# Performance work log

Measured on AMD Instinct MI355X. Metric: run time of the kernel, lower is better.

The kernel has to match this reference:

```python
import jax, jax.numpy as jnp
import numpy as np

NUM_SONGS = 2000
N1 = NUM_SONGS + 1  # incl. padding idx 0
EMB = 64
B = 32
S = 5    # num_prev_shows
M = 25   # max_songs_per_show


def setup_inputs() -> dict:
    key = jax.random.key(0)
    ks = jax.random.split(key, 32)
    def lin(k, i, o):
        kw, kb = jax.random.split(k)
        s = 1.0 / np.sqrt(i)
        return (jax.random.uniform(kw, (i, o), jnp.float32, -s, s),
                jax.random.uniform(kb, (o,), jnp.float32, -s, s))
    song_emb = jax.random.normal(ks[0], (N1, EMB), jnp.float32)
    song_emb = song_emb.at[0].set(0.0)  # padding_idx=0
    gcn_w1, gcn_b1 = lin(ks[1], EMB, EMB)
    gcn_w2, gcn_b2 = lin(ks[2], EMB, EMB)
    q_w, q_b = lin(ks[3], EMB, EMB)
    k_w, k_b = lin(ks[4], EMB, EMB)
    v_w, v_b = lin(ks[5], EMB, EMB)
    venue_t = jax.random.normal(ks[6], (200, EMB // 4), jnp.float32)
    tour_t = jax.random.normal(ks[7], (20, EMB // 4), jnp.float32)
    country_t = jax.random.normal(ks[8], (50, EMB // 8), jnp.float32)
    fest_t = jax.random.normal(ks[9], (2, EMB // 8), jnp.float32)
    mara_t = jax.random.normal(ks[10], (2, EMB // 8), jnp.float32)
    ctx_in = EMB // 2 + 3 * (EMB // 8)  # 56
    ctx_w, ctx_b = lin(ks[11], ctx_in, EMB)
    p1_w, p1_b = lin(ks[12], EMB * 3, EMB * 2)
    p2_w, p2_b = lin(ks[13], EMB * 2, EMB)
    p3_w, p3_b = lin(ks[14], EMB, 1)
    return {
        'song_ids': jax.random.randint(ks[20], (B,), 0, N1),
        'prev_setlists': jax.random.randint(ks[21], (B, S, M), 0, N1),
        'venue_ids': jax.random.randint(ks[22], (B,), 0, 200),
        'tour_ids': jax.random.randint(ks[23], (B,), 0, 20),
        'country_ids': jax.random.randint(ks[24], (B,), 0, 50),
        'is_festival': jax.random.randint(ks[25], (B,), 0, 2),
        'is_marathon': jax.random.randint(ks[26], (B,), 0, 2),
        'song_emb': song_emb,
        'gcn_w1': gcn_w1, 'gcn_b1': gcn_b1, 'gcn_w2': gcn_w2, 'gcn_b2': gcn_b2,
        'q_w': q_w, 'q_b': q_b, 'k_w': k_w, 'k_b': k_b, 'v_w': v_w, 'v_b': v_b,
        'venue_t': venue_t, 'tour_t': tour_t, 'country_t': country_t,
        'fest_t': fest_t, 'mara_t': mara_t,
        'ctx_w': ctx_w, 'ctx_b': ctx_b,
        'p1_w': p1_w, 'p1_b': p1_b, 'p2_w': p2_w, 'p2_b': p2_b,
        'p3_w': p3_w, 'p3_b': p3_b,
    }


def _build_adj(prev_setlists):
    # co-occurrence counts via one scatter-add (replaces nested python loops)
    b, s, m = prev_setlists.shape
    mask = prev_setlists > 0
    pair_ok = (mask[:, :, :, None] & mask[:, :, None, :]
               & ~jnp.eye(m, dtype=bool))  # exclude same position i==j
    flat_idx = (prev_setlists[:, :, :, None] * N1
                + prev_setlists[:, :, None, :]).reshape(b, -1)
    w = pair_ok.astype(jnp.float32).reshape(b, -1)
    adj = jnp.zeros((b, N1 * N1), jnp.float32)
    adj = adj.at[jnp.arange(b)[:, None], flat_idx].add(w)
    adj = adj.reshape(b, N1, N1)
    return adj / (adj.sum(axis=2, keepdims=True) + 1e-10)


def _forward(song_ids, prev_setlists, venue_ids, tour_ids, country_ids,
             is_festival, is_marathon, song_emb, gcn_w1, gcn_b1, gcn_w2,
             gcn_b2, q_w, q_b, k_w, k_b, v_w, v_b, venue_t, tour_t,
             country_t, fest_t, mara_t, ctx_w, ctx_b, p1_w, p1_b, p2_w,
             p2_b, p3_w, p3_b):
    b = song_ids.shape[0]
    adj = _build_adj(prev_setlists)                      # [B,N1,N1]
    x = jnp.broadcast_to(song_emb[None], (b, N1, EMB))   # [B,N1,E]
    for w_, b_ in ((gcn_w1, gcn_b1), (gcn_w2, gcn_b2)):
        agg = jnp.einsum('bnm,bme->bne', adj, x)
        x = jax.nn.relu(agg @ w_ + b_)
    song_embs = x
    # ragged masked-mean show embeddings
    mask = (prev_setlists > 0).astype(jnp.float32)       # [B,S,M]
    gathered = jax.vmap(lambda se, ids: se[ids])(song_embs, prev_setlists)  # [B,S,M,E]
    cnt = mask.sum(-1, keepdims=True)                    # [B,S,1]
    show_embs = jnp.where(cnt > 0,
                          (gathered * mask[..., None]).sum(2) / jnp.maximum(cnt, 1.0),
                          0.0)                           # [B,S,E]
    ctx = jnp.concatenate([venue_t[venue_ids], tour_t[tour_ids],
                           country_t[country_ids], fest_t[is_festival],
                           mara_t[is_marathon]], axis=-1)
    ctx = ctx @ ctx_w + ctx_b                            # [B,E]
    # temporal attention
    q = ctx @ q_w + q_b                                  # [B,E]
    k = show_embs @ k_w + k_b                            # [B,S,E]
    v = show_embs @ v_w + v_b
    scores = jnp.einsum('be,bse->bs', q, k) / jnp.sqrt(jnp.float32(EMB))
    attn = jax.nn.softmax(scores, axis=-1)
    attended = jnp.einsum('bs,bse->be', attn, v)
    cand = song_embs[jnp.arange(b), song_ids]
    h = jnp.concatenate([cand, ctx, attended], axis=-1)  # [B,3E]
    h = jax.nn.relu(h @ p1_w + p1_b)   # dropout is eval-mode identity
    h = jax.nn.relu(h @ p2_w + p2_b)
    logits = (h @ p3_w + p3_b).squeeze(-1)
    return jax.nn.sigmoid(logits)


def reference(song_ids, prev_setlists, venue_ids, tour_ids, country_ids,
              is_festival, is_marathon, song_emb, gcn_w1, gcn_b1, gcn_w2,
              gcn_b2, q_w, q_b, k_w, k_b, v_w, v_b, venue_t, tour_t,
              country_t, fest_t, mara_t, ctx_w, ctx_b, p1_w, p1_b, p2_w,
              p2_b, p3_w, p3_b):
    return _forward(song_ids, prev_setlists, venue_ids, tour_ids,
                    country_ids, is_festival, is_marathon, song_emb,
                    gcn_w1, gcn_b1, gcn_w2, gcn_b2, q_w, q_b, k_w, k_b,
                    v_w, v_b, venue_t, tour_t, country_t, fest_t, mara_t,
                    ctx_w, ctx_b, p1_w, p1_b, p2_w, p2_b, p3_w, p3_b)
```

## Files before the change

kernel.cpp:

```cpp
#include <hip/hip_runtime.h>

#define N1    2001
#define EMB   64
#define NSHOW 5
#define MSONG 25
#define NPOS  (NSHOW * MSONG)
#define MAXU  128
#define NT    1024
#define WT    68

__global__ __launch_bounds__(NT)
__attribute__((amdgpu_waves_per_eu(4, 4)))
void setsgnn_kernel(
    const int* __restrict__ song_ids,
    const int* __restrict__ prev_setlists,
    const int* __restrict__ venue_ids,
    const int* __restrict__ tour_ids,
    const int* __restrict__ country_ids,
    const int* __restrict__ is_festival,
    const int* __restrict__ is_marathon,
    const float* __restrict__ song_emb,
    const float* __restrict__ gcn_w1, const float* __restrict__ gcn_b1,
    const float* __restrict__ gcn_w2, const float* __restrict__ gcn_b2,
    const float* __restrict__ q_w,  const float* __restrict__ q_b,
    const float* __restrict__ k_w,  const float* __restrict__ k_b,
    const float* __restrict__ v_w,  const float* __restrict__ v_b,
    const float* __restrict__ venue_t, const float* __restrict__ tour_t,
    const float* __restrict__ country_t, const float* __restrict__ fest_t,
    const float* __restrict__ mara_t,
    const float* __restrict__ ctx_w, const float* __restrict__ ctx_b,
    const float* __restrict__ p1_w,  const float* __restrict__ p1_b,
    const float* __restrict__ p2_w,  const float* __restrict__ p2_b,
    const float* __restrict__ p3_w,  const float* __restrict__ p3_b,
    float* __restrict__ out)
{
    const int b    = blockIdx.x;
    const int tid  = threadIdx.x;
    const int wv   = tid >> 6;
    const int lane = tid & 63;
    const int col0 = tid & 63;
    const int eq0  = tid >> 6;

    __shared__ __align__(16) float xb0[MAXU][EMB];
    __shared__ __align__(16) float wldsT[2][EMB][WT];
    __shared__ __align__(16) float blds[2][EMB];
    __shared__ __align__(16) float bias_ctx[EMB], bias_q[EMB], bias_k[EMB], bias_v[EMB];
    __shared__ __align__(16) float bias_p1[128], bias_p2[EMB], bias_p3w[EMB];
    __shared__ float bias_p3b;
    __shared__ int   idmap[N1];
    __shared__ int   sl[NPOS];
    __shared__ int   pmap[NPOS];
    __shared__ int   list_ids[MAXU];
    __shared__ float c_us[MAXU][NSHOW];
    __shared__ float occv[MAXU];
    __shared__ float invv[MAXU];
    __shared__ float cntm1[NSHOW];
    __shared__ float invc[NSHOW];
    __shared__ int   U_cnt;
    __shared__ __align__(16) float Xsum[NSHOW][EMB];
    __shared__ float XW[NSHOW][EMB];
    __shared__ float ctxin[56];
    __shared__ float ctxv[EMB];
    __shared__ float qv[EMB];
    __shared__ float vatt[NSHOW][EMB];
    __shared__ float attnw[NSHOW];
    __shared__ float hbuf[3 * EMB];
    __shared__ float h1b[128];
    __shared__ float partial[NT];

    float w1r[4], w2r[4];
    #pragma unroll
    for (int j = 0; j < 4; j++) w1r[j] = gcn_w1[(eq0 * 4 + j) * EMB + col0];
    #pragma unroll
    for (int j = 0; j < 4; j++) w2r[j] = gcn_w2[(eq0 * 4 + j) * EMB + col0];
    float4 bb;
    if (tid < 32) bb = (tid < 16) ? ((const float4*)gcn_b1)[tid]
                                  : ((const float4*)gcn_b2)[tid - 16];
    const int slr = (tid < NPOS) ? prev_setlists[b * NPOS + tid] : 0;
    const int sid    = song_ids[b];
    const int vid    = venue_ids[b];
    const int tourid = tour_ids[b];
    const int cid    = country_ids[b];
    const int fid    = is_festival[b];
    const int mid    = is_marathon[b];

    for (int i = tid; i < N1; i += NT) idmap[i] = -1;
    if (tid < MAXU * NSHOW) ((float*)c_us)[tid] = 0.f;
    if (tid < NPOS) sl[tid] = slr;
    if (tid == 0) U_cnt = 0;
    *(float4*)&wldsT[0][col0][eq0 * 4] = make_float4(w1r[0], w1r[1], w1r[2], w1r[3]);
    *(float4*)&wldsT[1][col0][eq0 * 4] = make_float4(w2r[0], w2r[1], w2r[2], w2r[3]);
    if (tid < 32) ((float4*)blds)[tid] = bb;
    {
        int r = tid - 256;
        if (r >= 0 && r < 16)        ((float4*)bias_ctx)[r]       = ((const float4*)ctx_b)[r];
        else if (r >= 16 && r < 32)  ((float4*)bias_q)[r - 16]    = ((const float4*)q_b)[r - 16];
        else if (r >= 32 && r < 48)  ((float4*)bias_k)[r - 32]    = ((const float4*)k_b)[r - 32];
        else if (r >= 48 && r < 64)  ((float4*)bias_v)[r - 48]    = ((const float4*)v_b)[r - 48];
        else if (r >= 64 && r < 96)  ((float4*)bias_p1)[r - 64]   = ((const float4*)p1_b)[r - 64];
        else if (r >= 96 && r < 112) ((float4*)bias_p2)[r - 96]   = ((const float4*)p2_b)[r - 96];
        else if (r >= 112 && r < 128)((float4*)bias_p3w)[r - 112] = ((const float4*)p3_w)[r - 112];
        else if (r == 128)           bias_p3b = p3_b[0];
    }
    __syncthreads();

    if (tid < NPOS) {
        int id = sl[tid];
        if (id > 0) {
            if (atomicCAS(&idmap[id], -1, -2) == -1) {
                int u = atomicAdd(&U_cnt, 1);
                list_ids[u] = id;
                idmap[id] = u;
            }
        }
    } else if (tid == NPOS) {
        if (atomicCAS(&idmap[sid], -1, -2) == -1) {
            int u = atomicAdd(&U_cnt, 1);
            list_ids[u] = sid;
            idmap[sid] = u;
        }
    }
    if (tid >= 128 && tid < 128 + NSHOW) {
        int s = tid - 128, c = 0;
        for (int i = 0; i < MSONG; i++) c += (sl[s * MSONG + i] > 0) ? 1 : 0;
        cntm1[s] = (float)(c - 1);
        invc[s] = 1.f / fmaxf((float)c, 1.f);
    }
    if (tid >= 144 && tid < 200) {
        int e = tid - 144; float val;
        if (e < 16)      val = venue_t[vid * 16 + e];
        else if (e < 32) val = tour_t[tourid * 16 + (e - 16)];
        else if (e < 40) val = country_t[cid * 8 + (e - 32)];
        else if (e < 48) val = fest_t[fid * 8 + (e - 40)];
        else             val = mara_t[mid * 8 + (e - 48)];
        ctxin[e] = val;
    }
    if (wv >= 6 && wv < 11) {
        int s = wv - 6;
        float acc = 0.f;
        #pragma unroll
        for (int i = 0; i < MSONG; i++) {
            int id = sl[s * MSONG + i];
            if (id > 0) acc += song_emb[id * EMB + lane];
        }
        Xsum[s][lane] = acc;
    }
    __syncthreads();
    const int U = U_cnt;

    if (tid < NPOS) {
        int id = sl[tid];
        int pm = (id > 0) ? idmap[id] : -1;
        pmap[tid] = pm;
        if (pm >= 0) atomicAdd(&c_us[pm][tid / MSONG], 1.f);
    }
    if (tid >= 896 && tid < 960) {
        int c = tid - 896;
        float acc = bias_ctx[c];
        #pragma unroll
        for (int e = 0; e < 56; e++) acc += ctxin[e] * ctx_w[e * EMB + c];
        ctxv[c] = acc;
    }
    for (int t = tid; t < MAXU * (EMB / 4); t += NT) {
        int u = t >> 4, e4 = t & 15;
        float4 v = make_float4(0.f, 0.f, 0.f, 0.f);
        if (u < U) v = ((const float4*)(song_emb + list_ids[u] * EMB))[e4];
        *(float4*)&xb0[u][e4 * 4] = v;
    }
    __syncthreads();

    if (tid < MAXU) {
        float o = 0.f, r = 0.f;
        #pragma unroll
        for (int s = 0; s < NSHOW; s++) { float cc = c_us[tid][s]; o += cc; r += cc * cntm1[s]; }
        occv[tid] = o; invv[tid] = 1.f / (r + 1e-10f);
    }
    if (tid >= 128 && tid < 192) {
        int c = tid - 128;
        float acc = bias_q[c];
        #pragma unroll
        for (int e = 0; e < EMB; e++) acc += ctxv[e] * q_w[e * EMB + c];
        qv[c] = acc;
    }
    if (tid >= 192 && tid < 192 + NSHOW * EMB) {
        int t = tid - 192, s = t >> 6, c = t & 63;
        float acc = 0.f;
        #pragma unroll 4
        for (int e4 = 0; e4 < 16; e4++) {
            const float4 w4 = *(const float4*)&wldsT[0][c][e4 * 4];
            const float4 xs = *(const float4*)&Xsum[s][e4 * 4];
            acc += w4.x * xs.x + w4.y * xs.y + w4.z * xs.z + w4.w * xs.w;
        }
        XW[s][c] = acc;
    }
    __syncthreads();

    #define GCN_BODY(L)                                                          \
    {                                                                            \
        const float bias = blds[L][lane];                                        \
        float y[8];                                                              \
        _Pragma("unroll")                                                        \
        for (int uu = 0; uu < 8; ++uu) y[uu] = 0.f;                              \
        _Pragma("unroll 4")                                                      \
        for (int e4 = 0; e4 < 16; ++e4) {                                        \
            float4 a[8];                                                         \
            _Pragma("unroll")                                                    \
            for (int uu = 0; uu < 8; ++uu)                                       \
                a[uu] = *(const float4*)&xb0[(uu << 4) | wv][e4 * 4];            \
            const float4 w4 = *(const float4*)&wldsT[L][lane][e4 * 4];           \
            _Pragma("unroll")                                                    \
            for (int uu = 0; uu < 8; ++uu)                                       \
                y[uu] += a[uu].x * w4.x + a[uu].y * w4.y                         \
                       + a[uu].z * w4.z + a[uu].w * w4.w;                        \
        }                                                                        \
        _Pragma("unroll")                                                        \
        for (int uu = 0; uu < 8; ++uu) {                                         \
            const int u = (uu << 4) | wv;                                        \
            float acc = c_us[u][0] * XW[0][lane] + c_us[u][1] * XW[1][lane]      \
                      + c_us[u][2] * XW[2][lane] + c_us[u][3] * XW[3][lane]      \
                      + c_us[u][4] * XW[4][lane];                                \
            float val = (acc - occv[u] * y[uu]) * invv[u] + bias;                \
            xb0[u][lane] = fmaxf(val, 0.f);                                      \
        }                                                                        \
    }

    GCN_BODY(0)
    __syncthreads();

    {
        float kr[4];
        #pragma unroll
        for (int j = 0; j < 4; j++) kr[j] = k_w[(eq0 * 4 + j) * EMB + col0];
        if (wv >= 6 && wv < 11) {
            int s = wv - 6;
            int pm[MSONG];
            #pragma unroll
            for (int i = 0; i < MSONG; i++) pm[i] = pmap[s * MSONG + i];
            float acc = 0.f;
            #pragma unroll
            for (int i = 0; i < MSONG; i++) if (pm[i] >= 0) acc += xb0[pm[i]][lane];
            Xsum[s][lane] = acc;
        }
        *(float4*)&wldsT[0][col0][eq0 * 4] = make_float4(kr[0], kr[1], kr[2], kr[3]);
    }
    __syncthreads();

    if (tid >= 192 && tid < 192 + NSHOW * EMB) {
        int t = tid - 192, s = t >> 6, c = t & 63;
        float acc = 0.f;
        #pragma unroll 4
        for (int e4 = 0; e4 < 16; e4++) {
            const float4 w4 = *(const float4*)&wldsT[1][c][e4 * 4];
            const float4 xs = *(const float4*)&Xsum[s][e4 * 4];
            acc += w4.x * xs.x + w4.y * xs.y + w4.z * xs.z + w4.w * xs.w;
        }
        XW[s][c] = acc;
    }
    __syncthreads();

    float vr[4];
    #pragma unroll
    for (int j = 0; j < 4; j++) vr[j] = v_w[(eq0 * 4 + j) * EMB + col0];
    GCN_BODY(1)
    __syncthreads();

    *(float4*)&wldsT[1][col0][eq0 * 4] = make_float4(vr[0], vr[1], vr[2], vr[3]);
    const int kk1 = tid >> 7, o1 = tid & 127;
    const int kk2 = tid >> 6, o2 = lane;
    float p1wr[24], p2wr[8];
    #pragma unroll
    for (int j = 0; j < 24; j++) p1wr[j] = p1_w[(kk1 * 24 + j) * 128 + o1];
    #pragma unroll
    for (int j = 0; j < 8; j++)  p2wr[j] = p2_w[(kk2 * 8 + j) * 64 + o2];

    if (wv >= 6 && wv < 11) {
        int s = wv - 6;
        int pm[MSONG];
        #pragma unroll
        for (int i = 0; i < MSONG; i++) pm[i] = pmap[s * MSONG + i];
        float acc = 0.f;
        #pragma unroll
        for (int i = 0; i < MSONG; i++) if (pm[i] >= 0) acc += xb0[pm[i]][lane];
        Xsum[s][lane] = acc;
    }
    if (tid < 64)                    hbuf[tid] = xb0[idmap[sid]][tid];
    else if (tid >= 64 && tid < 128) hbuf[tid] = ctxv[tid - 64];
    __syncthreads();

    if (wv < NSHOW) {
        float s0 = 0.f;
        #pragma unroll 4
        for (int e4 = 0; e4 < 16; e4++) {
            const float4 w4 = *(const float4*)&wldsT[0][lane][e4 * 4];
            const float4 xs = *(const float4*)&Xsum[wv][e4 * 4];
            s0 += w4.x * xs.x + w4.y * xs.y + w4.z * xs.z + w4.w * xs.w;
        }
        float kk = s0 * invc[wv] + bias_k[lane];
        float p = kk * qv[lane];
        #pragma unroll
        for (int o = 32; o > 0; o >>= 1) p += __shfl_xor(p, o, 64);
        if (lane == 0) attnw[wv] = p * 0.125f;
    }
    if (wv >= 5 && wv < 10) {
        int s = wv - 5;
        float s0 = 0.f;
        #pragma unroll 4
        for (int e4 = 0; e4 < 16; e4++) {
            const float4 w4 = *(const float4*)&wldsT[1][lane][e4 * 4];
            const float4 xs = *(const float4*)&Xsum[s][e4 * 4];
            s0 += w4.x * xs.x + w4.y * xs.y + w4.z * xs.z + w4.w * xs.w;
        }
        vatt[s][lane] = s0 * invc[s] + bias_v[lane];
    }
    __syncthreads();

    if (wv == 0) {
        float a0 = attnw[0], a1 = attnw[1], a2 = attnw[2], a3 = attnw[3], a4 = attnw[4];
        float mx = fmaxf(fmaxf(fmaxf(a0, a1), fmaxf(a2, a3)), a4);
        float e0 = expf(a0 - mx), e1 = expf(a1 - mx), e2 = expf(a2 - mx),
              e3 = expf(a3 - mx), e4 = expf(a4 - mx);
        float isum = 1.f / (e0 + e1 + e2 + e3 + e4);
        float att = (e0 * vatt[0][lane] + e1 * vatt[1][lane] + e2 * vatt[2][lane]
                   + e3 * vatt[3][lane] + e4 * vatt[4][lane]) * isum;
        hbuf[2 * EMB + lane] = att;
    }
    __syncthreads();

    {
        float acc = (kk1 == 0) ? bias_p1[o1] : 0.f;
        #pragma unroll
        for (int j = 0; j < 24; j++) acc += hbuf[kk1 * 24 + j] * p1wr[j];
        partial[tid] = acc;
    }
    __syncthreads();

    if (tid < 128) {
        float acc = 0.f;
        #pragma unroll
        for (int kk = 0; kk < 8; kk++) acc += partial[kk * 128 + tid];
        h1b[tid] = fmaxf(acc, 0.f);
    }
    __syncthreads();

    {
        float acc = (kk2 == 0) ? bias_p2[o2] : 0.f;
        #pragma unroll
        for (int j = 0; j < 8; j++) acc += h1b[kk2 * 8 + j] * p2wr[j];
        partial[tid] = acc;
    }
    __syncthreads();

    if (wv == 0) {
        float acc = 0.f;
        #pragma unroll
        for (int kk = 0; kk < 16; kk++) acc += partial[kk * 64 + lane];
        float h2 = fmaxf(acc, 0.f);
        float p = h2 * bias_p3w[lane];
        #pragma unroll
        for (int o = 32; o > 0; o >>= 1) p += __shfl_xor(p, o, 64);
        if (lane == 0) out[b] = 1.f / (1.f + expf(-(p + bias_p3b)));
    }
}

extern "C" void kernel_launch(void* const* d_in, const int* in_sizes, int n_in,
                              void* d_out, int out_size, void* d_ws, size_t ws_size,
                              hipStream_t stream) {
    (void)n_in; (void)out_size; (void)d_ws; (void)ws_size;
    const int B = in_sizes[0];
    setsgnn_kernel<<<B, NT, 0, stream>>>(
        (const int*)d_in[0], (const int*)d_in[1], (const int*)d_in[2],
        (const int*)d_in[3], (const int*)d_in[4], (const int*)d_in[5],
        (const int*)d_in[6],
        (const float*)d_in[7],
        (const float*)d_in[8],  (const float*)d_in[9],
        (const float*)d_in[10], (const float*)d_in[11],
        (const float*)d_in[12], (const float*)d_in[13],
        (const float*)d_in[14], (const float*)d_in[15],
        (const float*)d_in[16], (const float*)d_in[17],
        (const float*)d_in[18], (const float*)d_in[19],
        (const float*)d_in[20], (const float*)d_in[21],
        (const float*)d_in[22],
        (const float*)d_in[23], (const float*)d_in[24],
        (const float*)d_in[25], (const float*)d_in[26],
        (const float*)d_in[27], (const float*)d_in[28],
        (const float*)d_in[29], (const float*)d_in[30],
        (float*)d_out);
}
```

Baseline: 33.67 us.

## Prefetch ctx/q weights to LDS, ballot-compact unique ids, sum Xsum from LDS

```diff
diff --git a/kernel.cpp b/kernel.cpp
--- a/kernel.cpp
+++ b/kernel.cpp
@@ -43,11 +43,13 @@
 
     __shared__ __align__(16) float xb0[MAXU][EMB];
     __shared__ __align__(16) float wldsT[2][EMB][WT];
+    __shared__ __align__(16) float ctxw_l[56][EMB];
+    __shared__ __align__(16) float qw_l[EMB][EMB];
     __shared__ __align__(16) float blds[2][EMB];
     __shared__ __align__(16) float bias_ctx[EMB], bias_q[EMB], bias_k[EMB], bias_v[EMB];
     __shared__ __align__(16) float bias_p1[128], bias_p2[EMB], bias_p3w[EMB];
     __shared__ float bias_p3b;
-    __shared__ int   idmap[N1];
+    __shared__ unsigned short idmap[N1];
     __shared__ int   sl[NPOS];
     __shared__ int   pmap[NPOS];
     __shared__ int   list_ids[MAXU];
@@ -73,6 +75,9 @@
     for (int j = 0; j < 4; j++) w1r[j] = gcn_w1[(eq0 * 4 + j) * EMB + col0];
     #pragma unroll
     for (int j = 0; j < 4; j++) w2r[j] = gcn_w2[(eq0 * 4 + j) * EMB + col0];
+    const float4 qw4 = ((const float4*)q_w)[tid];
+    float4 cw4 = make_float4(0.f, 0.f, 0.f, 0.f);
+    if (tid < 896) cw4 = ((const float4*)ctx_w)[tid];
     float4 bb;
     if (tid < 32) bb = (tid < 16) ? ((const float4*)gcn_b1)[tid]
                                   : ((const float4*)gcn_b2)[tid - 16];
@@ -84,12 +89,14 @@
     const int fid    = is_festival[b];
     const int mid    = is_marathon[b];
 
-    for (int i = tid; i < N1; i += NT) idmap[i] = -1;
+    for (int i = tid; i < N1; i += NT) idmap[i] = 0xFFFFu;
     if (tid < MAXU * NSHOW) ((float*)c_us)[tid] = 0.f;
     if (tid < NPOS) sl[tid] = slr;
     if (tid == 0) U_cnt = 0;
     *(float4*)&wldsT[0][col0][eq0 * 4] = make_float4(w1r[0], w1r[1], w1r[2], w1r[3]);
     *(float4*)&wldsT[1][col0][eq0 * 4] = make_float4(w2r[0], w2r[1], w2r[2], w2r[3]);
+    ((float4*)qw_l)[tid] = qw4;
+    if (tid < 896) ((float4*)ctxw_l)[tid] = cw4;
     if (tid < 32) ((float4*)blds)[tid] = bb;
     {
         int r = tid - 256;
@@ -104,22 +111,8 @@
     }
     __syncthreads();
 
-    if (tid < NPOS) {
-        int id = sl[tid];
-        if (id > 0) {
-            if (atomicCAS(&idmap[id], -1, -2) == -1) {
-                int u = atomicAdd(&U_cnt, 1);
-                list_ids[u] = id;
-                idmap[id] = u;
-            }
-        }
-    } else if (tid == NPOS) {
-        if (atomicCAS(&idmap[sid], -1, -2) == -1) {
-            int u = atomicAdd(&U_cnt, 1);
-            list_ids[u] = sid;
-            idmap[sid] = u;
-        }
-    }
+    if (tid < NPOS) { int id = sl[tid]; if (id > 0) idmap[id] = 1u; }
+    if (tid == NPOS) idmap[sid] = 1u;
     if (tid >= 128 && tid < 128 + NSHOW) {
         int s = tid - 128, c = 0;
         for (int i = 0; i < MSONG; i++) c += (sl[s * MSONG + i] > 0) ? 1 : 0;
@@ -135,22 +128,27 @@
         else             val = mara_t[mid * 8 + (e - 48)];
         ctxin[e] = val;
     }
-    if (wv >= 6 && wv < 11) {
-        int s = wv - 6;
-        float acc = 0.f;
-        #pragma unroll
-        for (int i = 0; i < MSONG; i++) {
-            int id = sl[s * MSONG + i];
-            if (id > 0) acc += song_emb[id * EMB + lane];
-        }
-        Xsum[s][lane] = acc;
+    __syncthreads();
+
+    for (int i = tid; i < N1; i += NT) {
+        const bool p = (idmap[i] == 1u);
+        const unsigned long long m = __ballot(p);
+        int base = 0;
+        if (lane == 0) { int c = __popcll(m); if (c) base = atomicAdd(&U_cnt, c); }
+        base = __shfl(base, 0, 64);
+        if (p) {
+            int r = __popcll(m & ((1ull << lane) - 1ull));
+            int u = base + r;
+            idmap[i] = (unsigned short)u;
+            list_ids[u] = i;
+        }
     }
     __syncthreads();
     const int U = U_cnt;
 
     if (tid < NPOS) {
         int id = sl[tid];
-        int pm = (id > 0) ? idmap[id] : -1;
+        int pm = (id > 0) ? (int)idmap[id] : -1;
         pmap[tid] = pm;
         if (pm >= 0) atomicAdd(&c_us[pm][tid / MSONG], 1.f);
     }
@@ -158,7 +156,7 @@
         int c = tid - 896;
         float acc = bias_ctx[c];
         #pragma unroll
-        for (int e = 0; e < 56; e++) acc += ctxin[e] * ctx_w[e * EMB + c];
+        for (int e = 0; e < 56; e++) acc += ctxin[e] * ctxw_l[e][c];
         ctxv[c] = acc;
     }
     for (int t = tid; t < MAXU * (EMB / 4); t += NT) {
@@ -179,11 +177,23 @@
         int c = tid - 128;
         float acc = bias_q[c];
         #pragma unroll
-        for (int e = 0; e < EMB; e++) acc += ctxv[e] * q_w[e * EMB + c];
+        for (int e = 0; e < EMB; e++) acc += ctxv[e] * qw_l[e][c];
         qv[c] = acc;
     }
-    if (tid >= 192 && tid < 192 + NSHOW * EMB) {
-        int t = tid - 192, s = t >> 6, c = t & 63;
+    if (wv >= 6 && wv < 11) {
+        int s = wv - 6;
+        int pm[MSONG];
+        #pragma unroll
+        for (int i = 0; i < MSONG; i++) pm[i] = pmap[s * MSONG + i];
+        float acc = 0.f;
+        #pragma unroll
+        for (int i = 0; i < MSONG; i++) if (pm[i] >= 0) acc += xb0[pm[i]][lane];
+        Xsum[s][lane] = acc;
+    }
+    __syncthreads();
+
+    if (tid < NSHOW * EMB) {
+        int s = tid >> 6, c = tid & 63;
         float acc = 0.f;
         #pragma unroll 4
         for (int e4 = 0; e4 < 16; e4++) {
@@ -245,8 +255,8 @@
     }
     __syncthreads();
 
-    if (tid >= 192 && tid < 192 + NSHOW * EMB) {
-        int t = tid - 192, s = t >> 6, c = t & 63;
+    if (tid < NSHOW * EMB) {
+        int s = tid >> 6, c = tid & 63;
         float acc = 0.f;
         #pragma unroll 4
         for (int e4 = 0; e4 < 16; e4++) {
@@ -283,7 +293,7 @@
         for (int i = 0; i < MSONG; i++) if (pm[i] >= 0) acc += xb0[pm[i]][lane];
         Xsum[s][lane] = acc;
     }
-    if (tid < 64)                    hbuf[tid] = xb0[idmap[sid]][tid];
+    if (tid < 64)                    hbuf[tid] = xb0[(int)idmap[sid]][tid];
     else if (tid >= 64 && tid < 128) hbuf[tid] = ctxv[tid - 64];
     __syncthreads();
 
```

After: 32.73 us. -2.8%, faster.
